# Kernel optimization log

Measured on AMD Instinct MI355X. Metric: run time of the kernel, lower is better.

Reference implementation:

```python
import jax, jax.numpy as jnp
import numpy as np


def setup_inputs() -> dict:
    key = jax.random.key(0)
    k1, k2, k3, k4 = jax.random.split(key, 4)
    B, T, C, H = 8, 2048, 768, 64
    x = jax.random.normal(k1, (B, T, C), dtype=jnp.float32)
    # nn.Linear(n_embd, head_size, bias=False): weight [H, C]; stored here as [C, H] for x @ W
    Wk = jax.random.normal(k2, (C, H), dtype=jnp.float32) * (C ** -0.5)
    Wq = jax.random.normal(k3, (C, H), dtype=jnp.float32) * (C ** -0.5)
    Wv = jax.random.normal(k4, (C, H), dtype=jnp.float32) * (C ** -0.5)
    return {"x": x, "Wk": Wk, "Wq": Wq, "Wv": Wv}


def reference(x, Wk, Wq, Wv):
    # x: [B, T, C]
    C = x.shape[-1]
    k = jnp.einsum("btc,ch->bth", x, Wk)  # [B, T, H]
    q = jnp.einsum("btc,ch->bth", x, Wq)  # [B, T, H]
    v = jnp.einsum("btc,ch->bth", x, Wv)  # [B, T, H]
    # NOTE: source scales by C**-0.5 where C = n_embd (input channels), not head_size
    wei = jnp.einsum("bth,bsh->bts", q, k) * (C ** -0.5)  # [B, T, T]
    wei = jax.nn.softmax(wei, axis=-1)
    # dropout p=0.0 (eval): identity
    out = jnp.einsum("bts,bsh->bth", wei, v)  # [B, T, H]
    return out
```

## Files before the change

### kernel.cpp

```cpp
#include <hip/hip_runtime.h>


typedef __attribute__((ext_vector_type(4))) float f32x4;
typedef __attribute__((ext_vector_type(8))) unsigned short u16x8;
typedef __attribute__((ext_vector_type(8))) __bf16 bf16x8;
typedef __attribute__((ext_vector_type(8))) _Float16 f16x8;

#define LDR 72
#define LDT 40
#define KSCALE (0.03608439182435161f * 1.4426950408889634f)
#define PBIAS 4.0f

typedef const __attribute__((address_space(1))) unsigned int* gas_u32p;
typedef __attribute__((address_space(3))) unsigned int* las_u32p;

__device__ __forceinline__ unsigned short f2bf(float f) {
  unsigned int u = __float_as_uint(f);
  u += 0x7FFFu + ((u >> 16) & 1u);
  return (unsigned short)(u >> 16);
}
__device__ __forceinline__ unsigned short hi16(float f) {
  return (unsigned short)(__float_as_uint(f) >> 16);
}
__device__ __forceinline__ f32x4 mfma_bf16(u16x8 a, u16x8 b, f32x4 c) {
  return __builtin_amdgcn_mfma_f32_16x16x32_bf16(
      __builtin_bit_cast(bf16x8, a), __builtin_bit_cast(bf16x8, b), c, 0, 0, 0);
}

__global__ __launch_bounds__(256) void wconv_k(const float* __restrict__ Wk,
                                               const float* __restrict__ Wq,
                                               const float* __restrict__ Wv,
                                               unsigned short* __restrict__ wt) {
  __shared__ unsigned short tr[64 * LDR];
  const int w = blockIdx.x / 12;
  const int kt = blockIdx.x - w * 12;
  const float* W = (w == 0) ? Wk : ((w == 1) ? Wq : Wv);
  const int tid = threadIdx.x;
  const int kr = tid >> 2;
  const int n0 = (tid & 3) * 16;
  const f32x4* src = (const f32x4*)(W + (size_t)(kt * 64 + kr) * 64 + n0);
  f32x4 a0 = src[0], a1 = src[1], a2 = src[2], a3 = src[3];
#pragma unroll
  for (int j = 0; j < 4; ++j) {
    tr[(n0 + j) * LDR + kr] = f2bf(a0[j]);
    tr[(n0 + 4 + j) * LDR + kr] = f2bf(a1[j]);
    tr[(n0 + 8 + j) * LDR + kr] = f2bf(a2[j]);
    tr[(n0 + 12 + j) * LDR + kr] = f2bf(a3[j]);
  }
  __syncthreads();
  const int n = tid >> 2, kc = (tid & 3) * 16;
  const int row = w * 64 + n;
  const int sw = (row & 7) << 4;
  unsigned short* tbase = wt + (size_t)kt * 12288 + row * 64;
#pragma unroll
  for (int jj = 0; jj < 2; ++jj) {
    const int j16 = kc * 2 + jj * 16;
    *(u16x8*)&tbase[(j16 ^ sw) >> 1] = *(const u16x8*)&tr[n * LDR + kc + jj * 8];
  }
}

__global__ __launch_bounds__(256) void proj_k(const float* __restrict__ x,
                                              const unsigned short* __restrict__ wt,
                                              unsigned short* __restrict__ kg,
                                              unsigned short* __restrict__ qg,
                                              unsigned short* __restrict__ vt) {
  __shared__ __align__(16) unsigned short x_s[32 * LDR];
  __shared__ __align__(16) unsigned short w_s[2][12288];
  __shared__ unsigned short vt_s[64 * LDT];
  const int tid = threadIdx.x;
  const int wv = tid >> 6, lane = tid & 63, c = lane & 15, quad = lane >> 4;
  const int m0 = blockIdx.x * 32;
  const int rowg = wv & 1;
  const int nfb = (wv >> 1) * 6;
  const int srow = tid >> 3;
  const int sc8 = (tid & 7) * 8;
  const int wsw = (c & 7) << 4;

  f32x4 acc[6];
#pragma unroll
  for (int i = 0; i < 6; ++i) acc[i] = f32x4{0.f, 0.f, 0.f, 0.f};

#pragma unroll
  for (int i = 0; i < 6; ++i)
    __builtin_amdgcn_global_load_lds(
        (gas_u32p)(const void*)(wt + i * 2048 + tid * 8),
        (las_u32p)(void*)(&w_s[0][i * 2048 + tid * 8]), 16, 0, 0);
  f32x4 xf0, xf1;
  {
    const f32x4* s = (const f32x4*)(x + (size_t)(m0 + srow) * 768 + sc8);
    xf0 = s[0]; xf1 = s[1];
  }

  for (int t = 0; t < 12; ++t) {
    {
      u16x8 u;
#pragma unroll
      for (int j = 0; j < 4; ++j) { u[j] = f2bf(xf0[j]); u[4 + j] = f2bf(xf1[j]); }
      *(u16x8*)&x_s[srow * LDR + sc8] = u;
    }
    asm volatile("s_waitcnt vmcnt(0)" ::: "memory");
    __syncthreads();
    if (t + 1 < 12) {
      const f32x4* s = (const f32x4*)(x + (size_t)(m0 + srow) * 768 + (t + 1) * 64 + sc8);
      xf0 = s[0]; xf1 = s[1];
      const unsigned short* wsrc = wt + (size_t)(t + 1) * 12288;
      unsigned short* wdst = w_s[(t + 1) & 1];
#pragma unroll
      for (int i = 0; i < 6; ++i)
        __builtin_amdgcn_global_load_lds(
            (gas_u32p)(const void*)(wsrc + i * 2048 + tid * 8),
            (las_u32p)(void*)(wdst + i * 2048 + tid * 8), 16, 0, 0);
    }
    const char* wp = (const char*)w_s[t & 1];
#pragma unroll
    for (int k32 = 0; k32 < 2; ++k32) {
      u16x8 a = *(const u16x8*)&x_s[(rowg * 16 + c) * LDR + k32 * 32 + quad * 8];
      const int koff = (k32 * 64 + quad * 16) ^ wsw;
#pragma unroll
      for (int j = 0; j < 6; ++j) {
        u16x8 b = *(const u16x8*)(wp + ((nfb + j) * 16 + c) * 128 + koff);
        acc[j] = mfma_bf16(a, b, acc[j]);
      }
    }
    __syncthreads();
  }
  const int r0 = rowg * 16 + quad * 4;
#pragma unroll
  for (int j = 0; j < 6; ++j) {
    const int nf = nfb + j;
    if (nf < 4) {
#pragma unroll
      for (int r = 0; r < 4; ++r)
        kg[(size_t)(m0 + r0 + r) * 64 + nf * 16 + c] = f2bf(acc[j][r]);
    } else if (nf < 8) {
#pragma unroll
      for (int r = 0; r < 4; ++r)
        qg[(size_t)(m0 + r0 + r) * 64 + (nf - 4) * 16 + c] = f2bf(acc[j][r] * KSCALE);
    } else {
#pragma unroll
      for (int r = 0; r < 4; ++r)
        vt_s[((nf - 8) * 16 + c) * LDT + r0 + r] = f2bf(acc[j][r]);
    }
  }
  __syncthreads();
  {
    const int h = tid >> 2, c8 = (tid & 3) * 8;
    const int b = m0 >> 11, tb = m0 & 2047;
    *(u16x8*)(vt + (size_t)b * 131072 + (size_t)h * 2048 + tb + c8) =
        *(const u16x8*)&vt_s[h * LDT + c8];
  }
}

__global__ __launch_bounds__(256, 4) void attn_k(const unsigned short* __restrict__ qg,
                                                 const unsigned short* __restrict__ kg,
                                                 const unsigned short* __restrict__ vt,
                                                 _Float16* __restrict__ part,
                                                 float* __restrict__ lsum) {
  __shared__ unsigned short k_s[64 * LDR];
  __shared__ unsigned short v_s[64 * LDR];
  __shared__ unsigned short p_s[64 * LDR];
  const int tid = threadIdx.x;
  const int wv = tid >> 6, lane = tid & 63, c = lane & 15, quad = lane >> 4;
  const int bq = blockIdx.x;
  const int qt = blockIdx.y;
  const int sc = blockIdx.z;
  const int tq0 = qt * 64;
  const int srow = tid >> 2, sch = (tid & 3) * 16;
  const int s_beg = sc << 9, s_end = s_beg + 512;

  const unsigned short* kbase = kg + (size_t)bq * 131072;
  const unsigned short* vbase = vt + (size_t)bq * 131072;

  u16x8 aq[2];
#pragma unroll
  for (int k32 = 0; k32 < 2; ++k32)
    aq[k32] = *(const u16x8*)(qg + (size_t)(bq * 2048 + tq0 + wv * 16 + c) * 64 +
                              k32 * 32 + quad * 8);

  u16x8 kb0 = *(const u16x8*)(kbase + (size_t)(s_beg + srow) * 64 + sch);
  u16x8 kb1 = *(const u16x8*)(kbase + (size_t)(s_beg + srow) * 64 + sch + 8);
  u16x8 vb0 = *(const u16x8*)(vbase + (size_t)srow * 2048 + s_beg + sch);
  u16x8 vb1 = *(const u16x8*)(vbase + (size_t)srow * 2048 + s_beg + sch + 8);

  u16x8 ones;
#pragma unroll
  for (int j = 0; j < 8; ++j) ones[j] = 0x3F80;

  f32x4 o_acc[4], l_acc;
#pragma unroll
  for (int hf = 0; hf < 4; ++hf) o_acc[hf] = f32x4{0.f, 0.f, 0.f, 0.f};
  l_acc = f32x4{0.f, 0.f, 0.f, 0.f};

  for (int s0 = s_beg; s0 < s_end; s0 += 64) {
    *(u16x8*)&k_s[srow * LDR + sch] = kb0;
    *(u16x8*)&k_s[srow * LDR + sch + 8] = kb1;
    *(u16x8*)&v_s[srow * LDR + sch] = vb0;
    *(u16x8*)&v_s[srow * LDR + sch + 8] = vb1;
    __syncthreads();
    if (s0 + 64 < s_end) {
      kb0 = *(const u16x8*)(kbase + (size_t)(s0 + 64 + srow) * 64 + sch);
      kb1 = *(const u16x8*)(kbase + (size_t)(s0 + 64 + srow) * 64 + sch + 8);
      vb0 = *(const u16x8*)(vbase + (size_t)srow * 2048 + s0 + 64 + sch);
      vb1 = *(const u16x8*)(vbase + (size_t)srow * 2048 + s0 + 64 + sch + 8);
    }
    f32x4 sacc[4];
#pragma unroll
    for (int nf = 0; nf < 4; ++nf) sacc[nf] = f32x4{0.f, 0.f, 0.f, 0.f};
#pragma unroll
    for (int k32 = 0; k32 < 2; ++k32) {
#pragma unroll
      for (int nf = 0; nf < 4; ++nf) {
        u16x8 b = *(const u16x8*)&k_s[(nf * 16 + c) * LDR + k32 * 32 + quad * 8];
        sacc[nf] = mfma_bf16(aq[k32], b, sacc[nf]);
      }
    }
    const int prow = wv * 16 + quad * 4;
#pragma unroll
    for (int nf = 0; nf < 4; ++nf)
#pragma unroll
      for (int r = 0; r < 4; ++r)
        p_s[(prow + r) * LDR + ((nf ^ quad) * 16) + c] =
            hi16(__builtin_amdgcn_exp2f(sacc[nf][r] - PBIAS));
    asm volatile("s_waitcnt lgkmcnt(0)" ::: "memory");
#pragma unroll
    for (int k32 = 0; k32 < 2; ++k32) {
      const int chunkP = (2 * k32 + (quad >> 1)) ^ (c >> 2);
      u16x8 ap = *(const u16x8*)&p_s[(wv * 16 + c) * LDR + chunkP * 16 + (quad & 1) * 8];
#pragma unroll
      for (int hf = 0; hf < 4; ++hf) {
        u16x8 bv = *(const u16x8*)&v_s[(hf * 16 + c) * LDR + k32 * 32 + quad * 8];
        o_acc[hf] = mfma_bf16(ap, bv, o_acc[hf]);
      }
      l_acc = mfma_bf16(ap, ones, l_acc);
    }
    __syncthreads();
  }
  const int pbase = (bq * 32 + qt) * 4 + sc;
  _Float16* po = part + (size_t)pbase * 4096;
#pragma unroll
  for (int hf = 0; hf < 4; ++hf)
#pragma unroll
    for (int r = 0; r < 4; ++r)
      po[(wv * 16 + quad * 4 + r) * 64 + hf * 16 + c] = (_Float16)o_acc[hf][r];
  if (c == 0) {
#pragma unroll
    for (int r = 0; r < 4; ++r)
      lsum[pbase * 64 + wv * 16 + quad * 4 + r] = l_acc[r];
  }
}

__global__ __launch_bounds__(256) void comb_k(const _Float16* __restrict__ part,
                                              const float* __restrict__ lsum,
                                              float* __restrict__ out) {
  const int bq = blockIdx.x, qh = blockIdx.y;
  const int qt = qh >> 1;
  const int row = (qh & 1) * 32 + (threadIdx.x >> 3);
  const int h0 = (threadIdx.x & 7) * 8;
  const int base = (bq * 32 + qt) * 4;
  float acc[8];
#pragma unroll
  for (int j = 0; j < 8; ++j) acc[j] = 0.f;
  float l = 0.f;
#pragma unroll
  for (int c4 = 0; c4 < 4; ++c4) {
    l += lsum[(base + c4) * 64 + row];
    f16x8 p = *(const f16x8*)(part + (size_t)(base + c4) * 4096 + row * 64 + h0);
#pragma unroll
    for (int j = 0; j < 8; ++j) acc[j] += (float)p[j];
  }
  const float inv = 1.0f / l;
  float* op = out + (size_t)(bq * 2048 + qt * 64 + row) * 64 + h0;
#pragma unroll
  for (int j = 0; j < 8; ++j) op[j] = acc[j] * inv;
}

extern "C" void kernel_launch(void* const* d_in, const int* in_sizes, int n_in,
                              void* d_out, int out_size, void* d_ws, size_t ws_size,
                              hipStream_t stream) {
  const float* x = (const float*)d_in[0];
  const float* Wk = (const float*)d_in[1];
  const float* Wq = (const float*)d_in[2];
  const float* Wv = (const float*)d_in[3];
  char* ws = (char*)d_ws;
  unsigned short* kg = (unsigned short*)(ws);
  unsigned short* qg = (unsigned short*)(ws + (size_t)(2 << 20));
  unsigned short* vt = (unsigned short*)(ws + (size_t)(4 << 20));
  unsigned short* wt = (unsigned short*)(ws + (size_t)(6 << 20));
  _Float16* part = (_Float16*)(ws + (size_t)(7 << 20));
  float* lsum = (float*)(ws + (size_t)(15 << 20));
  float* out = (float*)d_out;

  hipLaunchKernelGGL(wconv_k, dim3(36), dim3(256), 0, stream, Wk, Wq, Wv, wt);
  hipLaunchKernelGGL(proj_k, dim3(512), dim3(256), 0, stream, x, wt, kg, qg, vt);
  hipLaunchKernelGGL(attn_k, dim3(8, 32, 4), dim3(256), 0, stream, qg, kg, vt, part, lsum);
  hipLaunchKernelGGL(comb_k, dim3(8, 64), dim3(256), 0, stream, part, lsum, out);
}
```

Baseline: 122.3 us.

## Process two 64-row query groups per attention block to reuse K/V tiles

Each attention block now handles 128 query rows (two groups of 64) instead of 64. It shares each K/V tile loaded into LDS across twice as many MFMAs, which halves global K/V traffic and LDS staging per query. The trade-off is more registers (launch bounds drop to 2 blocks/CU), a larger P buffer in LDS, and half as many blocks (512), which may reduce occupancy and latency hiding. The combine kernel's indexing is adjusted to the new partial layout.

```diff
diff --git a/kernel.cpp b/kernel.cpp
--- a/kernel.cpp
+++ b/kernel.cpp
@@ -151,31 +151,33 @@
   }
 }
 
-__global__ __launch_bounds__(256, 4) void attn_k(const unsigned short* __restrict__ qg,
+__global__ __launch_bounds__(256, 2) void attn_k(const unsigned short* __restrict__ qg,
                                                  const unsigned short* __restrict__ kg,
                                                  const unsigned short* __restrict__ vt,
                                                  _Float16* __restrict__ part,
                                                  float* __restrict__ lsum) {
   __shared__ unsigned short k_s[64 * LDR];
   __shared__ unsigned short v_s[64 * LDR];
-  __shared__ unsigned short p_s[64 * LDR];
+  __shared__ unsigned short p_s[128 * LDR];
   const int tid = threadIdx.x;
   const int wv = tid >> 6, lane = tid & 63, c = lane & 15, quad = lane >> 4;
   const int bq = blockIdx.x;
   const int qt = blockIdx.y;
   const int sc = blockIdx.z;
-  const int tq0 = qt * 64;
+  const int tq0 = qt * 128;
   const int srow = tid >> 2, sch = (tid & 3) * 16;
   const int s_beg = sc << 9, s_end = s_beg + 512;
 
   const unsigned short* kbase = kg + (size_t)bq * 131072;
   const unsigned short* vbase = vt + (size_t)bq * 131072;
 
-  u16x8 aq[2];
-#pragma unroll
-  for (int k32 = 0; k32 < 2; ++k32)
-    aq[k32] = *(const u16x8*)(qg + (size_t)(bq * 2048 + tq0 + wv * 16 + c) * 64 +
-                              k32 * 32 + quad * 8);
+  u16x8 aq[2][2];
+#pragma unroll
+  for (int g = 0; g < 2; ++g)
+#pragma unroll
+    for (int k32 = 0; k32 < 2; ++k32)
+      aq[g][k32] = *(const u16x8*)(qg +
+          (size_t)(bq * 2048 + tq0 + g * 64 + wv * 16 + c) * 64 + k32 * 32 + quad * 8);
 
   u16x8 kb0 = *(const u16x8*)(kbase + (size_t)(s_beg + srow) * 64 + sch);
   u16x8 kb1 = *(const u16x8*)(kbase + (size_t)(s_beg + srow) * 64 + sch + 8);
@@ -186,10 +188,13 @@
 #pragma unroll
   for (int j = 0; j < 8; ++j) ones[j] = 0x3F80;
 
-  f32x4 o_acc[4], l_acc;
-#pragma unroll
-  for (int hf = 0; hf < 4; ++hf) o_acc[hf] = f32x4{0.f, 0.f, 0.f, 0.f};
-  l_acc = f32x4{0.f, 0.f, 0.f, 0.f};
+  f32x4 o_acc[2][4], l_acc[2];
+#pragma unroll
+  for (int g = 0; g < 2; ++g) {
+#pragma unroll
+    for (int hf = 0; hf < 4; ++hf) o_acc[g][hf] = f32x4{0.f, 0.f, 0.f, 0.f};
+    l_acc[g] = f32x4{0.f, 0.f, 0.f, 0.f};
+  }
 
   for (int s0 = s_beg; s0 < s_end; s0 += 64) {
     *(u16x8*)&k_s[srow * LDR + sch] = kb0;
@@ -203,49 +208,61 @@
       vb0 = *(const u16x8*)(vbase + (size_t)srow * 2048 + s0 + 64 + sch);
       vb1 = *(const u16x8*)(vbase + (size_t)srow * 2048 + s0 + 64 + sch + 8);
     }
-    f32x4 sacc[4];
-#pragma unroll
-    for (int nf = 0; nf < 4; ++nf) sacc[nf] = f32x4{0.f, 0.f, 0.f, 0.f};
+    f32x4 sacc[2][4];
+#pragma unroll
+    for (int g = 0; g < 2; ++g)
+#pragma unroll
+      for (int nf = 0; nf < 4; ++nf) sacc[g][nf] = f32x4{0.f, 0.f, 0.f, 0.f};
 #pragma unroll
     for (int k32 = 0; k32 < 2; ++k32) {
 #pragma unroll
       for (int nf = 0; nf < 4; ++nf) {
         u16x8 b = *(const u16x8*)&k_s[(nf * 16 + c) * LDR + k32 * 32 + quad * 8];
-        sacc[nf] = mfma_bf16(aq[k32], b, sacc[nf]);
+        sacc[0][nf] = mfma_bf16(aq[0][k32], b, sacc[0][nf]);
+        sacc[1][nf] = mfma_bf16(aq[1][k32], b, sacc[1][nf]);
       }
     }
     const int prow = wv * 16 + quad * 4;
 #pragma unroll
-    for (int nf = 0; nf < 4; ++nf)
-#pragma unroll
-      for (int r = 0; r < 4; ++r)
-        p_s[(prow + r) * LDR + ((nf ^ quad) * 16) + c] =
-            hi16(__builtin_amdgcn_exp2f(sacc[nf][r] - PBIAS));
+    for (int g = 0; g < 2; ++g)
+#pragma unroll
+      for (int nf = 0; nf < 4; ++nf)
+#pragma unroll
+        for (int r = 0; r < 4; ++r)
+          p_s[(g * 64 + prow + r) * LDR + ((nf ^ quad) * 16) + c] =
+              hi16(__builtin_amdgcn_exp2f(sacc[g][nf][r] - PBIAS));
     asm volatile("s_waitcnt lgkmcnt(0)" ::: "memory");
 #pragma unroll
     for (int k32 = 0; k32 < 2; ++k32) {
       const int chunkP = (2 * k32 + (quad >> 1)) ^ (c >> 2);
-      u16x8 ap = *(const u16x8*)&p_s[(wv * 16 + c) * LDR + chunkP * 16 + (quad & 1) * 8];
+      u16x8 ap0 = *(const u16x8*)&p_s[(wv * 16 + c) * LDR + chunkP * 16 + (quad & 1) * 8];
+      u16x8 ap1 = *(const u16x8*)&p_s[(64 + wv * 16 + c) * LDR + chunkP * 16 + (quad & 1) * 8];
 #pragma unroll
       for (int hf = 0; hf < 4; ++hf) {
         u16x8 bv = *(const u16x8*)&v_s[(hf * 16 + c) * LDR + k32 * 32 + quad * 8];
-        o_acc[hf] = mfma_bf16(ap, bv, o_acc[hf]);
+        o_acc[0][hf] = mfma_bf16(ap0, bv, o_acc[0][hf]);
+        o_acc[1][hf] = mfma_bf16(ap1, bv, o_acc[1][hf]);
       }
-      l_acc = mfma_bf16(ap, ones, l_acc);
+      l_acc[0] = mfma_bf16(ap0, ones, l_acc[0]);
+      l_acc[1] = mfma_bf16(ap1, ones, l_acc[1]);
     }
     __syncthreads();
   }
-  const int pbase = (bq * 32 + qt) * 4 + sc;
-  _Float16* po = part + (size_t)pbase * 4096;
-#pragma unroll
-  for (int hf = 0; hf < 4; ++hf)
-#pragma unroll
-    for (int r = 0; r < 4; ++r)
-      po[(wv * 16 + quad * 4 + r) * 64 + hf * 16 + c] = (_Float16)o_acc[hf][r];
-  if (c == 0) {
-#pragma unroll
-    for (int r = 0; r < 4; ++r)
-      lsum[pbase * 64 + wv * 16 + quad * 4 + r] = l_acc[r];
+  const int pbase = (bq * 16 + qt) * 4 + sc;
+  _Float16* po = part + (size_t)pbase * 8192;
+#pragma unroll
+  for (int g = 0; g < 2; ++g) {
+#pragma unroll
+    for (int hf = 0; hf < 4; ++hf)
+#pragma unroll
+      for (int r = 0; r < 4; ++r)
+        po[(g * 64 + wv * 16 + quad * 4 + r) * 64 + hf * 16 + c] =
+            (_Float16)o_acc[g][hf][r];
+    if (c == 0) {
+#pragma unroll
+      for (int r = 0; r < 4; ++r)
+        lsum[pbase * 128 + g * 64 + wv * 16 + quad * 4 + r] = l_acc[g][r];
+    }
   }
 }
 
@@ -253,23 +270,23 @@
                                               const float* __restrict__ lsum,
                                               float* __restrict__ out) {
   const int bq = blockIdx.x, qh = blockIdx.y;
-  const int qt = qh >> 1;
-  const int row = (qh & 1) * 32 + (threadIdx.x >> 3);
+  const int qt = qh >> 2;
+  const int row = (qh & 3) * 32 + (threadIdx.x >> 3);
   const int h0 = (threadIdx.x & 7) * 8;
-  const int base = (bq * 32 + qt) * 4;
+  const int base = (bq * 16 + qt) * 4;
   float acc[8];
 #pragma unroll
   for (int j = 0; j < 8; ++j) acc[j] = 0.f;
   float l = 0.f;
 #pragma unroll
   for (int c4 = 0; c4 < 4; ++c4) {
-    l += lsum[(base + c4) * 64 + row];
-    f16x8 p = *(const f16x8*)(part + (size_t)(base + c4) * 4096 + row * 64 + h0);
+    l += lsum[(base + c4) * 128 + row];
+    f16x8 p = *(const f16x8*)(part + (size_t)(base + c4) * 8192 + row * 64 + h0);
 #pragma unroll
     for (int j = 0; j < 8; ++j) acc[j] += (float)p[j];
   }
   const float inv = 1.0f / l;
-  float* op = out + (size_t)(bq * 2048 + qt * 64 + row) * 64 + h0;
+  float* op = out + (size_t)(bq * 2048 + qt * 128 + row) * 64 + h0;
 #pragma unroll
   for (int j = 0; j < 8; ++j) op[j] = acc[j] * inv;
 }
@@ -292,6 +309,6 @@
 
   hipLaunchKernelGGL(wconv_k, dim3(36), dim3(256), 0, stream, Wk, Wq, Wv, wt);
   hipLaunchKernelGGL(proj_k, dim3(512), dim3(256), 0, stream, x, wt, kg, qg, vt);
-  hipLaunchKernelGGL(attn_k, dim3(8, 32, 4), dim3(256), 0, stream, qg, kg, vt, part, lsum);
+  hipLaunchKernelGGL(attn_k, dim3(8, 16, 4), dim3(256), 0, stream, qg, kg, vt, part, lsum);
   hipLaunchKernelGGL(comb_k, dim3(8, 64), dim3(256), 0, stream, part, lsum, out);
 }
```

Result: no change. 120.3 us (-1.7%).
